# Performance work log

Measured on AMD Instinct MI355X. Metric: run time of the kernel, lower is better.

The kernel has to match this reference:

```python
import jax, jax.numpy as jnp
import numpy as np

# Profile-HMM forward-backward in log space.
# inputs : (M, B, L, S) soft/one-hot observation features
# log_A  : (M, Q, Q) row-stochastic log transition matrix
# log_pi : (M, Q)    log initial distribution
# log_B  : (M, Q, S) log emission matrix

M, B, L, Q, S = 1, 64, 2048, 256, 26
EPS = 1e-16


def setup_inputs() -> dict:
    key = jax.random.key(0)
    k1, k2, k3, k4 = jax.random.split(key, 4)
    inputs = jax.random.uniform(k1, (M, B, L, S), dtype=jnp.float32)
    log_A = jax.nn.log_softmax(jax.random.normal(k2, (M, Q, Q), dtype=jnp.float32), axis=-1)
    log_pi = jax.nn.log_softmax(jax.random.normal(k3, (M, Q), dtype=jnp.float32), axis=-1)
    log_B = jax.nn.log_softmax(jax.random.normal(k4, (M, Q, S), dtype=jnp.float32), axis=-1)
    return {"inputs": inputs, "log_A": log_A, "log_pi": log_pi, "log_B": log_B}


def _forward_backward(inputs, log_A, log_pi, log_B):
    # emission probs per state: e[m,b,l,q] = sum_s inputs[m,b,l,s] * B[m,q,s]
    emit = jnp.einsum('mbls,mqs->mblq', inputs, jnp.exp(log_B))
    log_e = jnp.log(emit + EPS)
    log_e_t = jnp.moveaxis(log_e, 2, 0)  # (L, M, B, Q) time-major

    # forward recursion: alpha_t[i] = logsumexp_j(alpha_{t-1}[j] + A[j,i]) + e_t[i]
    alpha0 = log_pi[:, None, :] + log_e_t[0]  # (M, B, Q)

    def fstep(alpha, le):
        new = jax.nn.logsumexp(alpha[..., :, None] + log_A[:, None], axis=-2) + le
        return new, new

    _, alphas = jax.lax.scan(fstep, alpha0, log_e_t[1:])
    alphas = jnp.concatenate([alpha0[None], alphas], axis=0)  # (L, M, B, Q)

    # backward recursion: beta_t[i] = logsumexp_j(A[i,j] + e_{t+1}[j] + beta_{t+1}[j])
    beta_last = jnp.zeros_like(alpha0)

    def bstep(beta, le):
        new = jax.nn.logsumexp(log_A[:, None] + (le + beta)[:, :, None, :], axis=-1)
        return new, new

    _, betas = jax.lax.scan(bstep, beta_last, log_e_t[1:], reverse=True)
    betas = jnp.concatenate([betas, beta_last[None]], axis=0)  # (L, M, B, Q)

    loglik = jax.nn.logsumexp(alphas[-1], axis=-1)  # (M, B)
    post = alphas + betas - loglik[None, :, :, None]  # state posterior log probs
    return jnp.moveaxis(post, 0, 2), loglik  # (M, B, L, Q), (M, B)


def reference(inputs, log_A, log_pi, log_B):
    post, loglik = _forward_backward(inputs, log_A, log_pi, log_B)
    return post, loglik
```

## Files before the change

### kernel.cpp

```cpp
#include <hip/hip_runtime.h>

namespace {

constexpr int B = 64;
constexpr int L = 2048;
constexpr int Q = 256;
constexpr int S = 26;
constexpr float EPS = 1e-16f;
constexpr size_t POST = (size_t)B * L * Q;

typedef _Float16 h2 __attribute__((ext_vector_type(2)));
typedef _Float16 f16x8 __attribute__((ext_vector_type(8)));
typedef float f32x4 __attribute__((ext_vector_type(4)));

#define MFMA16(a, b, c) __builtin_amdgcn_mfma_f32_16x16x32_f16((a), (b), (c), 0, 0, 0)

struct Smem {
  alignas(16) _Float16 vb[2][Q];
  alignas(16) _Float16 rowh[2][32];
  alignas(16) _Float16 rowl[2][32];
  float sh[2];
  alignas(16) float afin[Q];
};

__device__ __forceinline__ void lds_barrier() {
  asm volatile("s_waitcnt lgkmcnt(0)\n\ts_barrier" ::: "memory");
}

__device__ __forceinline__ float wave_max64(float x) {
#pragma unroll
  for (int off = 32; off > 0; off >>= 1) x = fmaxf(x, __shfl_xor(x, off, 64));
  return x;
}
__device__ __forceinline__ float wave_sum64(float x) {
#pragma unroll
  for (int off = 32; off > 0; off >>= 1) x += __shfl_xor(x, off, 64);
  return x;
}

__device__ __forceinline__ void load_emit_frags(const float* __restrict__ log_B,
                                                int c0, int c1, int g, int q,
                                                f16x8& Bh0, f16x8& Bl0,
                                                f16x8& Bh1, f16x8& Bl1) {
#pragma unroll
  for (int j = 0; j < 8; ++j) {
    const int s = g * 8 + j;
    const float v0 = (s < S) ? __expf(log_B[(size_t)(c0 + q) * S + s]) : 0.f;
    const float v1 = (s < S) ? __expf(log_B[(size_t)(c1 + q) * S + s]) : 0.f;
    const _Float16 h0 = (_Float16)v0, h1 = (_Float16)v1;
    Bh0[j] = h0; Bl0[j] = (_Float16)(v0 - (float)h0);
    Bh1[j] = h1; Bl1[j] = (_Float16)(v1 - (float)h1);
  }
}

__device__ __forceinline__ void stage_row(Smem& sm, int buf, int lane, float2 gg) {
  _Float16 ah = (_Float16)0.f, bh = (_Float16)0.f;
  _Float16 al = (_Float16)0.f, bl = (_Float16)0.f;
  if (lane < 13) {
    ah = (_Float16)gg.x; bh = (_Float16)gg.y;
    al = (_Float16)(gg.x - (float)ah);
    bl = (_Float16)(gg.y - (float)bh);
  }
  ((h2*)sm.rowh[buf])[lane] = h2{ah, bh};
  ((h2*)sm.rowl[buf])[lane] = h2{al, bl};
}

__device__ __forceinline__ void emit_mfma(const f16x8& xh, const f16x8& xl,
                                          const f16x8& Bh0, const f16x8& Bl0,
                                          const f16x8& Bh1, const f16x8& Bl1,
                                          f32x4& E0, f32x4& E1) {
  const f32x4 Z = {0.f, 0.f, 0.f, 0.f};
  E0 = MFMA16(xh, Bl0, Z);
  E0 = MFMA16(xl, Bh0, E0);
  E0 = MFMA16(xh, Bh0, E0);
  E1 = MFMA16(xh, Bl1, Z);
  E1 = MFMA16(xl, Bh1, E1);
  E1 = MFMA16(xh, Bh1, E1);
}

__device__ __forceinline__ void matvec_mfma(const f16x8* va, const f16x8* T0,
                                            const f16x8* T1, float& x0, float& x1) {
  const f32x4 Z = {0.f, 0.f, 0.f, 0.f};
  f32x4 X0a = MFMA16(va[0], T0[0], Z);
  f32x4 X1a = MFMA16(va[0], T1[0], Z);
  f32x4 X0b = MFMA16(va[4], T0[4], Z);
  f32x4 X1b = MFMA16(va[4], T1[4], Z);
#pragma unroll
  for (int f = 1; f < 4; ++f) {
    X0a = MFMA16(va[f], T0[f], X0a);
    X1a = MFMA16(va[f], T1[f], X1a);
    X0b = MFMA16(va[f + 4], T0[f + 4], X0b);
    X1b = MFMA16(va[f + 4], T1[f + 4], X1b);
  }
  x0 = X0a[0] + X0b[0];
  x1 = X1a[0] + X1b[0];
}

__device__ __forceinline__ void read_frags(Smem& sm, int p, int g,
                                           f16x8& xh, f16x8& xl, f16x8* va) {
  xh = *(const f16x8*)(sm.rowh[p] + g * 8);
  xl = *(const f16x8*)(sm.rowl[p] + g * 8);
  const _Float16* vbp = sm.vb[p];
#pragma unroll
  for (int f = 0; f < 8; ++f) va[f] = *(const f16x8*)(vbp + f * 32 + g * 8);
}

__device__ __forceinline__ void fwd_impl(int b, const float* __restrict__ inputs,
                                         const float* __restrict__ log_A,
                                         const float* __restrict__ log_pi,
                                         const float* __restrict__ log_B,
                                         float* __restrict__ out, Smem& sm) {
  const int tid = threadIdx.x, w = tid >> 6, lane = tid & 63;
  const int g = lane >> 4, q = lane & 15;
  const int c0 = w * 32, c1 = c0 + 16;
  const bool rdl = (q == 0);
  const bool epi = (lane < 16);
  const bool stg = (w == 0) && (lane < 16);

  f16x8 T0[8], T1[8];
#pragma unroll
  for (int f = 0; f < 8; ++f) {
#pragma unroll
    for (int j = 0; j < 8; ++j) {
      const int k = f * 32 + g * 8 + j;
      T0[f][j] = (_Float16)__expf(log_A[(size_t)k * Q + c0 + q]);
      T1[f][j] = (_Float16)__expf(log_A[(size_t)k * Q + c1 + q]);
    }
  }
  f16x8 Bh0, Bl0, Bh1, Bl1;
  load_emit_frags(log_B, c0, c1, g, q, Bh0, Bl0, Bh1, Bl1);

  const float2* __restrict__ inp2 = (const float2*)(inputs + (size_t)b * L * S);
  float* __restrict__ post_b = out + (size_t)b * L * Q;

  float2 gHold = {0.f, 0.f};
  if (stg) {
    float2 g0 = {0.f, 0.f}, g1 = {0.f, 0.f};
    if (lane < 13) {
      g0 = inp2[lane];
      g1 = inp2[13 + lane];
      gHold = inp2[26 + lane];
    }
    stage_row(sm, 1, lane, g0);
    stage_row(sm, 0, lane, g1);
  }
  __syncthreads();

  f16x8 xh = {}, xl = {};
  f16x8 va[8];
#pragma unroll
  for (int f = 0; f < 8; ++f) va[f] = f16x8{};

  if (rdl) {
    xh = *(const f16x8*)(sm.rowh[1] + g * 8);
    xl = *(const f16x8*)(sm.rowl[1] + g * 8);
  }
  f32x4 E0, E1;
  emit_mfma(xh, xl, Bh0, Bl0, Bh1, Bl1, E0, E1);
  float zh0 = 1.f, zh1 = 1.f, rdp_h = 0.f;
  if (epi) {
    zh0 = (E0[0] + EPS) * __expf(log_pi[c0 + lane]);
    zh1 = (E1[0] + EPS) * __expf(log_pi[c1 + lane]);
  }
  if (tid == 0) sm.sh[0] = __logf(zh0);
  __syncthreads();
  float rd_prev = sm.sh[0];
  if (epi) {
    const float sc = __expf(-rd_prev);
    sm.vb[0][c0 + lane] = (_Float16)(zh0 * sc);
    sm.vb[0][c1 + lane] = (_Float16)(zh1 * sc);
  }
  __syncthreads();

  int p = 0;
  for (int t = 1; t < L; ++t) {
    if (stg) stage_row(sm, p ^ 1, lane, gHold);
    const float rd = sm.sh[p];
    float2 gN = gHold;
    const int tt = (t + 2 < L) ? t + 2 : L - 1;
    if (w == 0 && lane < 13) gN = inp2[(size_t)tt * 13 + lane];
    if (epi) {
      const float a0 = __logf(zh0) + rdp_h;
      const float a1 = __logf(zh1) + rdp_h;
      post_b[(size_t)(t - 1) * Q + c0 + lane] = a0;
      post_b[(size_t)(t - 1) * Q + c1 + lane] = a1;
    }
    if (rdl) read_frags(sm, p, g, xh, xl, va);
    f32x4 E0_, E1_;
    emit_mfma(xh, xl, Bh0, Bl0, Bh1, Bl1, E0_, E1_);
    float x0, x1;
    matvec_mfma(va, T0, T1, x0, x1);
    const float gam = __expf(rd_prev - rd);
    if (epi) {
      const float e0 = E0_[0] + EPS, e1 = E1_[0] + EPS;
      const float z0 = x0 * e0, z1 = x1 * e1;
      sm.vb[p ^ 1][c0 + lane] = (_Float16)(z0 * gam);
      sm.vb[p ^ 1][c1 + lane] = (_Float16)(z1 * gam);
      if (tid == 0) sm.sh[p ^ 1] = __logf(z0) + rd_prev;
      zh0 = z0; zh1 = z1;
    }
    gHold = gN;
    rdp_h = rd_prev;
    rd_prev = rd;
    lds_barrier();
    p ^= 1;
  }

  if (epi) {
    const float a0 = __logf(zh0) + rdp_h;
    const float a1 = __logf(zh1) + rdp_h;
    post_b[(size_t)(L - 1) * Q + c0 + lane] = a0;
    post_b[(size_t)(L - 1) * Q + c1 + lane] = a1;
    sm.afin[c0 + lane] = a0;
    sm.afin[c1 + lane] = a1;
  }
  __syncthreads();
  if (w == 0) {
    float4 fa = ((const float4*)sm.afin)[lane];
    float m = fmaxf(fmaxf(fa.x, fa.y), fmaxf(fa.z, fa.w));
    m = wave_max64(m);
    float ss = __expf(fa.x - m) + __expf(fa.y - m) + __expf(fa.z - m) + __expf(fa.w - m);
    ss = wave_sum64(ss);
    if (lane == 0) out[POST + b] = __logf(ss) + m;
  }
}

template <int MODE>
__device__ __forceinline__ void bwd_impl(int b, const float* __restrict__ inputs,
                                         const float* __restrict__ log_A,
                                         const float* __restrict__ log_B,
                                         float* __restrict__ out,
                                         float* __restrict__ ws, Smem& sm) {
  const int tid = threadIdx.x, w = tid >> 6, lane = tid & 63;
  const int g = lane >> 4, q = lane & 15;
  const int c0 = w * 32, c1 = c0 + 16;
  const bool rdl = (q == 0);
  const bool epi = (lane < 16);
  const bool stg = (w == 0) && (lane < 16);

  f16x8 T0[8], T1[8];
#pragma unroll
  for (int f = 0; f < 8; ++f) {
#pragma unroll
    for (int j = 0; j < 8; ++j) {
      const int k = f * 32 + g * 8 + j;
      T0[f][j] = (_Float16)__expf(log_A[(size_t)(c0 + q) * Q + k]);
      T1[f][j] = (_Float16)__expf(log_A[(size_t)(c1 + q) * Q + k]);
    }
  }
  f16x8 Bh0, Bl0, Bh1, Bl1;
  load_emit_frags(log_B, c0, c1, g, q, Bh0, Bl0, Bh1, Bl1);

  const float2* __restrict__ inp2 = (const float2*)(inputs + (size_t)b * L * S);
  float* __restrict__ post_b = out + (size_t)b * L * Q;
  float* __restrict__ ws_b = ws + (size_t)b * L * Q;

  float ll = 0.f, a_h0 = 0.f, a_h1 = 0.f;
  if (MODE == 1) {
    ll = out[POST + b];
    if (epi) {
      a_h0 = post_b[(size_t)(L - 1) * Q + c0 + lane];
      a_h1 = post_b[(size_t)(L - 1) * Q + c1 + lane];
    }
  }

  float2 gHold = {0.f, 0.f};
  if (stg) {
    float2 g0 = {0.f, 0.f}, g1 = {0.f, 0.f};
    if (lane < 13) {
      g0 = inp2[(size_t)(L - 1) * 13 + lane];
      g1 = inp2[(size_t)(L - 2) * 13 + lane];
      gHold = inp2[(size_t)(L - 3) * 13 + lane];
    }
    stage_row(sm, 1, lane, g0);
    stage_row(sm, 0, lane, g1);
  }
  __syncthreads();

  f16x8 xh = {}, xl = {};
  f16x8 va[8];
#pragma unroll
  for (int f = 0; f < 8; ++f) va[f] = f16x8{};

  if (rdl) {
    xh = *(const f16x8*)(sm.rowh[1] + g * 8);
    xl = *(const f16x8*)(sm.rowl[1] + g * 8);
  }
  f32x4 E0, E1;
  emit_mfma(xh, xl, Bh0, Bl0, Bh1, Bl1, E0, E1);
  float e0i = 1.f, e1i = 1.f;
  if (epi) { e0i = E0[0] + EPS; e1i = E1[0] + EPS; }
  if (tid == 0) sm.sh[0] = __logf(e0i);
  __syncthreads();
  float rd_prev = sm.sh[0];
  if (epi) {
    const float sc = __expf(-rd_prev);
    sm.vb[0][c0 + lane] = (_Float16)(e0i * sc);
    sm.vb[0][c1 + lane] = (_Float16)(e1i * sc);
  }
  float rh0 = 1.f, rh1 = 1.f, rdp_h = 0.f;
  __syncthreads();

  int p = 0;
  for (int t = L - 2; t >= 0; --t) {
    if (stg) stage_row(sm, p ^ 1, lane, gHold);
    const float rd = sm.sh[p];
    float2 gN = gHold;
    const int tt = (t >= 2) ? t - 2 : 0;
    if (w == 0 && lane < 13) gN = inp2[(size_t)tt * 13 + lane];
    if (epi) {
      const float b0 = __logf(rh0) + rdp_h;
      const float b1 = __logf(rh1) + rdp_h;
      if (MODE == 0) {
        ws_b[(size_t)(t + 1) * Q + c0 + lane] = b0;
        ws_b[(size_t)(t + 1) * Q + c1 + lane] = b1;
      } else {
        post_b[(size_t)(t + 1) * Q + c0 + lane] = a_h0 + b0 - ll;
        post_b[(size_t)(t + 1) * Q + c1 + lane] = a_h1 + b1 - ll;
        a_h0 = post_b[(size_t)t * Q + c0 + lane];
        a_h1 = post_b[(size_t)t * Q + c1 + lane];
      }
    }
    if (rdl) read_frags(sm, p, g, xh, xl, va);
    f32x4 E0_, E1_;
    emit_mfma(xh, xl, Bh0, Bl0, Bh1, Bl1, E0_, E1_);
    float r0, r1;
    matvec_mfma(va, T0, T1, r0, r1);
    const float gam = __expf(rd_prev - rd);
    if (epi) {
      const float e0 = E0_[0] + EPS, e1 = E1_[0] + EPS;
      const float z0 = r0 * e0, z1 = r1 * e1;
      sm.vb[p ^ 1][c0 + lane] = (_Float16)(z0 * gam);
      sm.vb[p ^ 1][c1 + lane] = (_Float16)(z1 * gam);
      if (tid == 0) sm.sh[p ^ 1] = __logf(z0) + rd_prev;
      rh0 = r0; rh1 = r1;
    }
    gHold = gN;
    rdp_h = rd_prev;
    rd_prev = rd;
    lds_barrier();
    p ^= 1;
  }

  if (epi) {
    const float b0 = __logf(rh0) + rdp_h;
    const float b1 = __logf(rh1) + rdp_h;
    if (MODE == 0) {
      ws_b[c0 + lane] = b0;
      ws_b[c1 + lane] = b1;
    } else {
      post_b[c0 + lane] = a_h0 + b0 - ll;
      post_b[c1 + lane] = a_h1 + b1 - ll;
    }
  }
}

__global__ __launch_bounds__(512, 2)
void hmm_fwdbwd(const float* __restrict__ inputs, const float* __restrict__ log_A,
                const float* __restrict__ log_pi, const float* __restrict__ log_B,
                float* __restrict__ out, float* __restrict__ ws) {
  __shared__ Smem sm;
  if (blockIdx.x < B) fwd_impl(blockIdx.x, inputs, log_A, log_pi, log_B, out, sm);
  else                bwd_impl<0>(blockIdx.x - B, inputs, log_A, log_B, out, ws, sm);
}

__global__ __launch_bounds__(256)
void hmm_combine(const float* __restrict__ ws, float* __restrict__ out) {
  const size_t idx = (size_t)blockIdx.x * 256 + threadIdx.x;
  const int b = (int)(idx >> 17);
  const float ll = out[POST + b];
  float4 a = ((const float4*)out)[idx];
  const float4 be = ((const float4*)ws)[idx];
  a.x += be.x - ll;
  a.y += be.y - ll;
  a.z += be.z - ll;
  a.w += be.w - ll;
  ((float4*)out)[idx] = a;
}

__global__ __launch_bounds__(512, 2)
void hmm_fwd_only(const float* __restrict__ inputs, const float* __restrict__ log_A,
                  const float* __restrict__ log_pi, const float* __restrict__ log_B,
                  float* __restrict__ out) {
  __shared__ Smem sm;
  fwd_impl(blockIdx.x, inputs, log_A, log_pi, log_B, out, sm);
}

__global__ __launch_bounds__(512, 2)
void hmm_bwd_fused(const float* __restrict__ inputs, const float* __restrict__ log_A,
                   const float* __restrict__ log_B, float* __restrict__ out) {
  __shared__ Smem sm;
  bwd_impl<1>(blockIdx.x, inputs, log_A, log_B, out, nullptr, sm);
}

}

extern "C" void kernel_launch(void* const* d_in, const int* in_sizes, int n_in,
                              void* d_out, int out_size, void* d_ws, size_t ws_size,
                              hipStream_t stream) {
  const float* inputs = (const float*)d_in[0];
  const float* log_A  = (const float*)d_in[1];
  const float* log_pi = (const float*)d_in[2];
  const float* log_B  = (const float*)d_in[3];
  float* out = (float*)d_out;
  float* ws  = (float*)d_ws;

  if (ws_size >= POST * sizeof(float)) {
    hipLaunchKernelGGL(hmm_fwdbwd, dim3(2 * B), dim3(512), 0, stream,
                       inputs, log_A, log_pi, log_B, out, ws);
    hipLaunchKernelGGL(hmm_combine, dim3((unsigned)(POST / 4 / 256)), dim3(256), 0, stream,
                       ws, out);
  } else {
    hipLaunchKernelGGL(hmm_fwd_only, dim3(B), dim3(512), 0, stream,
                       inputs, log_A, log_pi, log_B, out);
    hipLaunchKernelGGL(hmm_bwd_fused, dim3(B), dim3(512), 0, stream,
                       inputs, log_A, log_B, out);
  }
}
```

Before: 1.601 ms.

## Software-pipeline emission MFMA one step ahead and shorten matvec dependency chains

Computes the emission probabilities for step t+1 during step t, so the emit MFMAs sit off the critical recurrence path and the product uses the value computed in the previous iteration. The prologue loads the first two input rows straight from global memory, converts them in registers, and drops one __syncthreads, and the staged-row prefetch now runs one step further ahead. The matvec is split into four independent accumulation chains of two MFMAs instead of two chains of four, cutting serial MFMA latency. Pointer-increment addressing replaces per-step index arithmetic. The cost is extra live registers for the pipelined values and a more intricate prologue.

```diff
diff --git a/kernel.cpp b/kernel.cpp
--- a/kernel.cpp
+++ b/kernel.cpp
@@ -63,6 +63,25 @@
   }
   ((h2*)sm.rowh[buf])[lane] = h2{ah, bh};
   ((h2*)sm.rowl[buf])[lane] = h2{al, bl};
+}
+
+__device__ __forceinline__ void load_row(const float2* __restrict__ r2, int g,
+                                         bool rdl, float2* ld) {
+  if (rdl) {
+    const float2* p = r2 + g * 4;
+    ld[0] = p[0];
+    if (g < 3) { ld[1] = p[1]; ld[2] = p[2]; ld[3] = p[3]; }
+  }
+}
+
+__device__ __forceinline__ void cvt_row(const float2* ld, f16x8& xh, f16x8& xl) {
+#pragma unroll
+  for (int i = 0; i < 4; ++i) {
+    const float a = ld[i].x, bb = ld[i].y;
+    const _Float16 ah = (_Float16)a, bh = (_Float16)bb;
+    xh[2 * i] = ah;     xl[2 * i] = (_Float16)(a - (float)ah);
+    xh[2 * i + 1] = bh; xl[2 * i + 1] = (_Float16)(bb - (float)bh);
+  }
 }
 
 __device__ __forceinline__ void emit_mfma(const f16x8& xh, const f16x8& xl,
@@ -78,22 +97,19 @@
   E1 = MFMA16(xh, Bh1, E1);
 }
 
-__device__ __forceinline__ void matvec_mfma(const f16x8* va, const f16x8* T0,
-                                            const f16x8* T1, float& x0, float& x1) {
+__device__ __forceinline__ void matvec2(const f16x8* va, const f16x8* T0,
+                                        const f16x8* T1, float& x0, float& x1) {
   const f32x4 Z = {0.f, 0.f, 0.f, 0.f};
-  f32x4 X0a = MFMA16(va[0], T0[0], Z);
-  f32x4 X1a = MFMA16(va[0], T1[0], Z);
-  f32x4 X0b = MFMA16(va[4], T0[4], Z);
-  f32x4 X1b = MFMA16(va[4], T1[4], Z);
-#pragma unroll
-  for (int f = 1; f < 4; ++f) {
-    X0a = MFMA16(va[f], T0[f], X0a);
-    X1a = MFMA16(va[f], T1[f], X1a);
-    X0b = MFMA16(va[f + 4], T0[f + 4], X0b);
-    X1b = MFMA16(va[f + 4], T1[f + 4], X1b);
-  }
-  x0 = X0a[0] + X0b[0];
-  x1 = X1a[0] + X1b[0];
+  f32x4 a0 = MFMA16(va[0], T0[0], Z); a0 = MFMA16(va[1], T0[1], a0);
+  f32x4 b0 = MFMA16(va[2], T0[2], Z); b0 = MFMA16(va[3], T0[3], b0);
+  f32x4 c0 = MFMA16(va[4], T0[4], Z); c0 = MFMA16(va[5], T0[5], c0);
+  f32x4 d0 = MFMA16(va[6], T0[6], Z); d0 = MFMA16(va[7], T0[7], d0);
+  f32x4 a1 = MFMA16(va[0], T1[0], Z); a1 = MFMA16(va[1], T1[1], a1);
+  f32x4 b1 = MFMA16(va[2], T1[2], Z); b1 = MFMA16(va[3], T1[3], b1);
+  f32x4 c1 = MFMA16(va[4], T1[4], Z); c1 = MFMA16(va[5], T1[5], c1);
+  f32x4 d1 = MFMA16(va[6], T1[6], Z); d1 = MFMA16(va[7], T1[7], d1);
+  x0 = (a0[0] + b0[0]) + (c0[0] + d0[0]);
+  x1 = (a1[0] + b1[0]) + (c1[0] + d1[0]);
 }
 
 __device__ __forceinline__ void read_frags(Smem& sm, int p, int g,
@@ -131,32 +147,27 @@
   load_emit_frags(log_B, c0, c1, g, q, Bh0, Bl0, Bh1, Bl1);
 
   const float2* __restrict__ inp2 = (const float2*)(inputs + (size_t)b * L * S);
+  const float2* __restrict__ rlast = inp2 + (size_t)(L - 1) * 13;
   float* __restrict__ post_b = out + (size_t)b * L * Q;
 
-  float2 gHold = {0.f, 0.f};
-  if (stg) {
-    float2 g0 = {0.f, 0.f}, g1 = {0.f, 0.f};
-    if (lane < 13) {
-      g0 = inp2[lane];
-      g1 = inp2[13 + lane];
-      gHold = inp2[26 + lane];
-    }
-    stage_row(sm, 1, lane, g0);
-    stage_row(sm, 0, lane, g1);
-  }
-  __syncthreads();
+  float2 r0v[4] = {}, r1v[4] = {};
+  load_row(inp2, g, rdl, r0v);
+  load_row(inp2 + 13, g, rdl, r1v);
+  float2 g2 = {0.f, 0.f}, gHold = {0.f, 0.f};
+  if (w == 0 && lane < 13) { g2 = inp2[26 + lane]; gHold = inp2[39 + lane]; }
+  if (stg) stage_row(sm, 0, lane, g2);
 
   f16x8 xh = {}, xl = {};
-  f16x8 va[8];
-#pragma unroll
-  for (int f = 0; f < 8; ++f) va[f] = f16x8{};
-
-  if (rdl) {
-    xh = *(const f16x8*)(sm.rowh[1] + g * 8);
-    xl = *(const f16x8*)(sm.rowl[1] + g * 8);
-  }
+  cvt_row(r0v, xh, xl);
   f32x4 E0, E1;
   emit_mfma(xh, xl, Bh0, Bl0, Bh1, Bl1, E0, E1);
+  float eP0, eP1;
+  {
+    cvt_row(r1v, xh, xl);
+    f32x4 F0, F1;
+    emit_mfma(xh, xl, Bh0, Bl0, Bh1, Bl1, F0, F1);
+    eP0 = F0[0] + EPS; eP1 = F1[0] + EPS;
+  }
   float zh0 = 1.f, zh1 = 1.f, rdp_h = 0.f;
   if (epi) {
     zh0 = (E0[0] + EPS) * __expf(log_pi[c0 + lane]);
@@ -172,33 +183,38 @@
   }
   __syncthreads();
 
+  f16x8 va[8];
+#pragma unroll
+  for (int f = 0; f < 8; ++f) va[f] = f16x8{};
+
+  const float2* pin = inp2 + 4 * 13;
+  float* pb = post_b + c0 + lane;
   int p = 0;
   for (int t = 1; t < L; ++t) {
     if (stg) stage_row(sm, p ^ 1, lane, gHold);
     const float rd = sm.sh[p];
+    if (rdl) read_frags(sm, p, g, xh, xl, va);
     float2 gN = gHold;
-    const int tt = (t + 2 < L) ? t + 2 : L - 1;
-    if (w == 0 && lane < 13) gN = inp2[(size_t)tt * 13 + lane];
+    if (w == 0 && lane < 13) gN = ((t + 3 < L) ? pin : rlast)[lane];
+    pin += 13;
     if (epi) {
-      const float a0 = __logf(zh0) + rdp_h;
-      const float a1 = __logf(zh1) + rdp_h;
-      post_b[(size_t)(t - 1) * Q + c0 + lane] = a0;
-      post_b[(size_t)(t - 1) * Q + c1 + lane] = a1;
-    }
-    if (rdl) read_frags(sm, p, g, xh, xl, va);
-    f32x4 E0_, E1_;
-    emit_mfma(xh, xl, Bh0, Bl0, Bh1, Bl1, E0_, E1_);
+      pb[0]  = __logf(zh0) + rdp_h;
+      pb[16] = __logf(zh1) + rdp_h;
+    }
+    pb += Q;
+    f32x4 F0_, F1_;
+    emit_mfma(xh, xl, Bh0, Bl0, Bh1, Bl1, F0_, F1_);
     float x0, x1;
-    matvec_mfma(va, T0, T1, x0, x1);
+    matvec2(va, T0, T1, x0, x1);
     const float gam = __expf(rd_prev - rd);
     if (epi) {
-      const float e0 = E0_[0] + EPS, e1 = E1_[0] + EPS;
-      const float z0 = x0 * e0, z1 = x1 * e1;
+      const float z0 = x0 * eP0, z1 = x1 * eP1;
       sm.vb[p ^ 1][c0 + lane] = (_Float16)(z0 * gam);
       sm.vb[p ^ 1][c1 + lane] = (_Float16)(z1 * gam);
       if (tid == 0) sm.sh[p ^ 1] = __logf(z0) + rd_prev;
       zh0 = z0; zh1 = z1;
     }
+    eP0 = F0_[0] + EPS; eP1 = F1_[0] + EPS;
     gHold = gN;
     rdp_h = rd_prev;
     rd_prev = rd;
@@ -209,8 +225,7 @@
   if (epi) {
     const float a0 = __logf(zh0) + rdp_h;
     const float a1 = __logf(zh1) + rdp_h;
-    post_b[(size_t)(L - 1) * Q + c0 + lane] = a0;
-    post_b[(size_t)(L - 1) * Q + c1 + lane] = a1;
+    pb[0] = a0; pb[16] = a1;
     sm.afin[c0 + lane] = a0;
     sm.afin[c1 + lane] = a1;
   }
@@ -264,30 +279,27 @@
     }
   }
 
-  float2 gHold = {0.f, 0.f};
-  if (stg) {
-    float2 g0 = {0.f, 0.f}, g1 = {0.f, 0.f};
-    if (lane < 13) {
-      g0 = inp2[(size_t)(L - 1) * 13 + lane];
-      g1 = inp2[(size_t)(L - 2) * 13 + lane];
-      gHold = inp2[(size_t)(L - 3) * 13 + lane];
-    }
-    stage_row(sm, 1, lane, g0);
-    stage_row(sm, 0, lane, g1);
-  }
-  __syncthreads();
+  float2 rAv[4] = {}, rBv[4] = {};
+  load_row(inp2 + (size_t)(L - 1) * 13, g, rdl, rAv);
+  load_row(inp2 + (size_t)(L - 2) * 13, g, rdl, rBv);
+  float2 g2 = {0.f, 0.f}, gHold = {0.f, 0.f};
+  if (w == 0 && lane < 13) {
+    g2 = inp2[(size_t)(L - 3) * 13 + lane];
+    gHold = inp2[(size_t)(L - 4) * 13 + lane];
+  }
+  if (stg) stage_row(sm, 0, lane, g2);
 
   f16x8 xh = {}, xl = {};
-  f16x8 va[8];
-#pragma unroll
-  for (int f = 0; f < 8; ++f) va[f] = f16x8{};
-
-  if (rdl) {
-    xh = *(const f16x8*)(sm.rowh[1] + g * 8);
-    xl = *(const f16x8*)(sm.rowl[1] + g * 8);
-  }
+  cvt_row(rAv, xh, xl);
   f32x4 E0, E1;
   emit_mfma(xh, xl, Bh0, Bl0, Bh1, Bl1, E0, E1);
+  float eP0, eP1;
+  {
+    cvt_row(rBv, xh, xl);
+    f32x4 F0, F1;
+    emit_mfma(xh, xl, Bh0, Bl0, Bh1, Bl1, F0, F1);
+    eP0 = F0[0] + EPS; eP1 = F1[0] + EPS;
+  }
   float e0i = 1.f, e1i = 1.f;
   if (epi) { e0i = E0[0] + EPS; e1i = E1[0] + EPS; }
   if (tid == 0) sm.sh[0] = __logf(e0i);
@@ -301,40 +313,47 @@
   float rh0 = 1.f, rh1 = 1.f, rdp_h = 0.f;
   __syncthreads();
 
+  f16x8 va[8];
+#pragma unroll
+  for (int f = 0; f < 8; ++f) va[f] = f16x8{};
+
+  const float2* pin = inp2 + (size_t)(L - 5) * 13;
+  float* wp = ws_b + (size_t)(L - 1) * Q + c0 + lane;
+  float* pp = post_b + (size_t)(L - 1) * Q + c0 + lane;
   int p = 0;
   for (int t = L - 2; t >= 0; --t) {
     if (stg) stage_row(sm, p ^ 1, lane, gHold);
     const float rd = sm.sh[p];
+    if (rdl) read_frags(sm, p, g, xh, xl, va);
     float2 gN = gHold;
-    const int tt = (t >= 2) ? t - 2 : 0;
-    if (w == 0 && lane < 13) gN = inp2[(size_t)tt * 13 + lane];
+    if (w == 0 && lane < 13) gN = ((t >= 3) ? pin : inp2)[lane];
+    pin -= 13;
     if (epi) {
       const float b0 = __logf(rh0) + rdp_h;
       const float b1 = __logf(rh1) + rdp_h;
       if (MODE == 0) {
-        ws_b[(size_t)(t + 1) * Q + c0 + lane] = b0;
-        ws_b[(size_t)(t + 1) * Q + c1 + lane] = b1;
+        wp[0] = b0; wp[16] = b1;
       } else {
-        post_b[(size_t)(t + 1) * Q + c0 + lane] = a_h0 + b0 - ll;
-        post_b[(size_t)(t + 1) * Q + c1 + lane] = a_h1 + b1 - ll;
-        a_h0 = post_b[(size_t)t * Q + c0 + lane];
-        a_h1 = post_b[(size_t)t * Q + c1 + lane];
+        pp[0] = a_h0 + b0 - ll;
+        pp[16] = a_h1 + b1 - ll;
+        a_h0 = (pp - Q)[0];
+        a_h1 = (pp - Q)[16];
       }
     }
-    if (rdl) read_frags(sm, p, g, xh, xl, va);
-    f32x4 E0_, E1_;
-    emit_mfma(xh, xl, Bh0, Bl0, Bh1, Bl1, E0_, E1_);
+    wp -= Q; pp -= Q;
+    f32x4 F0_, F1_;
+    emit_mfma(xh, xl, Bh0, Bl0, Bh1, Bl1, F0_, F1_);
     float r0, r1;
-    matvec_mfma(va, T0, T1, r0, r1);
+    matvec2(va, T0, T1, r0, r1);
     const float gam = __expf(rd_prev - rd);
     if (epi) {
-      const float e0 = E0_[0] + EPS, e1 = E1_[0] + EPS;
-      const float z0 = r0 * e0, z1 = r1 * e1;
+      const float z0 = r0 * eP0, z1 = r1 * eP1;
       sm.vb[p ^ 1][c0 + lane] = (_Float16)(z0 * gam);
       sm.vb[p ^ 1][c1 + lane] = (_Float16)(z1 * gam);
       if (tid == 0) sm.sh[p ^ 1] = __logf(z0) + rd_prev;
       rh0 = r0; rh1 = r1;
     }
+    eP0 = F0_[0] + EPS; eP1 = F1_[0] + EPS;
     gHold = gN;
     rdp_h = rd_prev;
     rd_prev = rd;
@@ -346,11 +365,10 @@
     const float b0 = __logf(rh0) + rdp_h;
     const float b1 = __logf(rh1) + rdp_h;
     if (MODE == 0) {
-      ws_b[c0 + lane] = b0;
-      ws_b[c1 + lane] = b1;
+      wp[0] = b0; wp[16] = b1;
     } else {
-      post_b[c0 + lane] = a_h0 + b0 - ll;
-      post_b[c1 + lane] = a_h1 + b1 - ll;
+      pp[0] = a_h0 + b0 - ll;
+      pp[16] = a_h1 + b1 - ll;
     }
   }
 }
```

New measurement: 1.683 ms. 5.1% more time.

## Precompute emissions in separate parallel kernel before forward/backward recursion

Applied to the files above, without the earlier changes.

Adds an hmm_emit kernel that computes all emission probabilities with split-fp16 MFMA across 256 blocks and stores them as fp16 in workspace. The forward/backward recursion kernels then only load the precomputed per-timestep emissions, which removes the per-step emission matmul from the serial critical path. The path runs only when the workspace holds 6 bytes per posterior element. It costs an extra launch and a round trip of the emission tensor through global memory, and fp16 storage with a clamp at 6e-5 changes precision for very small emissions.

```diff
diff --git a/kernel.cpp b/kernel.cpp
--- a/kernel.cpp
+++ b/kernel.cpp
@@ -14,6 +14,332 @@
 typedef float f32x4 __attribute__((ext_vector_type(4)));
 
 #define MFMA16(a, b, c) __builtin_amdgcn_mfma_f32_16x16x32_f16((a), (b), (c), 0, 0, 0)
+
+
+__device__ __forceinline__ void lds_barrier() {
+  asm volatile("s_waitcnt lgkmcnt(0)\n\ts_barrier" ::: "memory");
+}
+
+__device__ __forceinline__ float wave_max64(float x) {
+#pragma unroll
+  for (int off = 32; off > 0; off >>= 1) x = fmaxf(x, __shfl_xor(x, off, 64));
+  return x;
+}
+__device__ __forceinline__ float wave_sum64(float x) {
+#pragma unroll
+  for (int off = 32; off > 0; off >>= 1) x += __shfl_xor(x, off, 64);
+  return x;
+}
+
+
+struct SmemE {
+  alignas(16) _Float16 vb[2][Q];
+  float sh[2];
+  alignas(16) float afin[Q];
+};
+
+__device__ __forceinline__ void matvec2(const f16x8* va, const f16x8* T0,
+                                        const f16x8* T1, float& x0, float& x1) {
+  const f32x4 Z = {0.f, 0.f, 0.f, 0.f};
+  f32x4 a0 = MFMA16(va[0], T0[0], Z); a0 = MFMA16(va[1], T0[1], a0);
+  f32x4 b0 = MFMA16(va[2], T0[2], Z); b0 = MFMA16(va[3], T0[3], b0);
+  f32x4 c0 = MFMA16(va[4], T0[4], Z); c0 = MFMA16(va[5], T0[5], c0);
+  f32x4 d0 = MFMA16(va[6], T0[6], Z); d0 = MFMA16(va[7], T0[7], d0);
+  f32x4 a1 = MFMA16(va[0], T1[0], Z); a1 = MFMA16(va[1], T1[1], a1);
+  f32x4 b1 = MFMA16(va[2], T1[2], Z); b1 = MFMA16(va[3], T1[3], b1);
+  f32x4 c1 = MFMA16(va[4], T1[4], Z); c1 = MFMA16(va[5], T1[5], c1);
+  f32x4 d1 = MFMA16(va[6], T1[6], Z); d1 = MFMA16(va[7], T1[7], d1);
+  x0 = (a0[0] + b0[0]) + (c0[0] + d0[0]);
+  x1 = (a1[0] + b1[0]) + (c1[0] + d1[0]);
+}
+
+__device__ __forceinline__ void read_va(SmemE& sm, int p, int g, f16x8* va) {
+  const _Float16* vbp = sm.vb[p];
+#pragma unroll
+  for (int f = 0; f < 8; ++f) va[f] = *(const f16x8*)(vbp + f * 32 + g * 8);
+}
+
+__global__ __launch_bounds__(512)
+void hmm_emit(const float* __restrict__ inputs, const float* __restrict__ log_B,
+              _Float16* __restrict__ eall) {
+  const int tid = threadIdx.x, w = tid >> 6, lane = tid & 63;
+  const int g = lane >> 4, q = lane & 15;
+  const int b = blockIdx.x >> 2, quar = blockIdx.x & 3;
+  const float* __restrict__ inp = inputs + (size_t)b * L * S;
+  _Float16* __restrict__ eb = eall + (size_t)b * L * Q;
+
+  const int tbase = (quar * 32 + w * 4) * 16;
+  f16x8 xh[4], xl[4];
+#pragma unroll
+  for (int i = 0; i < 4; ++i) {
+    const int trow = tbase + i * 16 + q;
+    const float* rp = inp + (size_t)trow * S;
+    float v[8];
+#pragma unroll
+    for (int j = 0; j < 8; ++j) {
+      const int s = g * 8 + j;
+      v[j] = (s < S) ? rp[s] : 0.f;
+    }
+#pragma unroll
+    for (int j = 0; j < 8; ++j) {
+      const _Float16 h = (_Float16)v[j];
+      xh[i][j] = h;
+      xl[i][j] = (_Float16)(v[j] - (float)h);
+    }
+  }
+  for (int k = 0; k < 16; ++k) {
+    f16x8 Bh, Bl;
+#pragma unroll
+    for (int j = 0; j < 8; ++j) {
+      const int s = g * 8 + j;
+      const float vv = (s < S) ? __expf(log_B[(size_t)(k * 16 + q) * S + s]) : 0.f;
+      const _Float16 h = (_Float16)vv;
+      Bh[j] = h;
+      Bl[j] = (_Float16)(vv - (float)h);
+    }
+    const f32x4 Z = {0.f, 0.f, 0.f, 0.f};
+#pragma unroll
+    for (int i = 0; i < 4; ++i) {
+      f32x4 E = MFMA16(xh[i], Bl, Z);
+      E = MFMA16(xl[i], Bh, E);
+      E = MFMA16(xh[i], Bh, E);
+      const int t0 = tbase + i * 16 + (lane >> 4) * 4;
+      const int col = k * 16 + (lane & 15);
+#pragma unroll
+      for (int r = 0; r < 4; ++r) {
+        const float ev = fmaxf(E[r] + EPS, 6.0e-5f);
+        eb[(size_t)(t0 + r) * Q + col] = (_Float16)ev;
+      }
+    }
+  }
+}
+
+__device__ __forceinline__ void fwd_e(int b, const _Float16* __restrict__ eall,
+                                      const float* __restrict__ log_A,
+                                      const float* __restrict__ log_pi,
+                                      float* __restrict__ out, SmemE& sm) {
+  const int tid = threadIdx.x, w = tid >> 6, lane = tid & 63;
+  const int g = lane >> 4, q = lane & 15;
+  const int c0 = w * 32, c1 = c0 + 16;
+  const bool rdl = (q == 0);
+  const bool epi = (lane < 16);
+
+  f16x8 T0[8], T1[8];
+#pragma unroll
+  for (int f = 0; f < 8; ++f) {
+#pragma unroll
+    for (int j = 0; j < 8; ++j) {
+      const int k = f * 32 + g * 8 + j;
+      T0[f][j] = (_Float16)__expf(log_A[(size_t)k * Q + c0 + q]);
+      T1[f][j] = (_Float16)__expf(log_A[(size_t)k * Q + c1 + q]);
+    }
+  }
+
+  const _Float16* __restrict__ eb = eall + (size_t)b * L * Q;
+  float* __restrict__ post_b = out + (size_t)b * L * Q;
+  const _Float16* e0p = eb + c0 + lane;
+
+  float ez0 = 1.f, ez1 = 1.f;
+  float e1a = 1.f, e1b = 1.f, e2a = 1.f, e2b = 1.f;
+  float e3a = 1.f, e3b = 1.f, e0a = 1.f, e0b = 1.f;
+  if (epi) {
+    ez0 = (float)e0p[0];        ez1 = (float)e0p[16];
+    e1a = (float)e0p[1 * Q];    e1b = (float)e0p[1 * Q + 16];
+    e2a = (float)e0p[2 * Q];    e2b = (float)e0p[2 * Q + 16];
+    e3a = (float)e0p[3 * Q];    e3b = (float)e0p[3 * Q + 16];
+    e0a = (float)e0p[4 * Q];    e0b = (float)e0p[4 * Q + 16];
+  }
+
+  float zh0 = 1.f, zh1 = 1.f, rdp_h = 0.f;
+  if (epi) {
+    zh0 = ez0 * __expf(log_pi[c0 + lane]);
+    zh1 = ez1 * __expf(log_pi[c1 + lane]);
+  }
+  if (tid == 0) sm.sh[0] = __logf(zh0);
+  __syncthreads();
+  float rd_prev = sm.sh[0];
+  if (epi) {
+    const float sc = __expf(-rd_prev);
+    sm.vb[0][c0 + lane] = (_Float16)(zh0 * sc);
+    sm.vb[0][c1 + lane] = (_Float16)(zh1 * sc);
+  }
+  __syncthreads();
+
+  f16x8 va[8];
+#pragma unroll
+  for (int f = 0; f < 8; ++f) va[f] = f16x8{};
+
+  const _Float16* ep = eb + (size_t)5 * Q + c0 + lane;
+  const _Float16* epLast = eb + (size_t)(L - 1) * Q + c0 + lane;
+  float* pb = post_b + c0 + lane;
+  int p = 0;
+
+  auto step = [&](float& eX0, float& eX1) {
+    const float rd = sm.sh[p];
+    if (rdl) read_va(sm, p, g, va);
+    if (epi) {
+      pb[0] = __logf(zh0) + rdp_h;
+      pb[16] = __logf(zh1) + rdp_h;
+    }
+    pb += Q;
+    float x0, x1;
+    matvec2(va, T0, T1, x0, x1);
+    const float gam = __expf(rd_prev - rd);
+    if (epi) {
+      const float z0 = x0 * eX0, z1 = x1 * eX1;
+      sm.vb[p ^ 1][c0 + lane] = (_Float16)(z0 * gam);
+      sm.vb[p ^ 1][c1 + lane] = (_Float16)(z1 * gam);
+      if (tid == 0) sm.sh[p ^ 1] = __logf(z0) + rd_prev;
+      zh0 = z0; zh1 = z1;
+      const _Float16* pe = (ep <= epLast) ? ep : epLast;
+      eX0 = (float)pe[0];
+      eX1 = (float)pe[16];
+    }
+    ep += Q;
+    rdp_h = rd_prev;
+    rd_prev = rd;
+    lds_barrier();
+    p ^= 1;
+  };
+
+  int t = 1;
+  for (; t + 3 < L; t += 4) {
+    step(e1a, e1b);
+    step(e2a, e2b);
+    step(e3a, e3b);
+    step(e0a, e0b);
+  }
+  step(e1a, e1b);
+  step(e2a, e2b);
+  step(e3a, e3b);
+
+  if (epi) {
+    const float a0 = __logf(zh0) + rdp_h;
+    const float a1 = __logf(zh1) + rdp_h;
+    pb[0] = a0; pb[16] = a1;
+    sm.afin[c0 + lane] = a0;
+    sm.afin[c1 + lane] = a1;
+  }
+  __syncthreads();
+  if (w == 0) {
+    float4 fa = ((const float4*)sm.afin)[lane];
+    float m = fmaxf(fmaxf(fa.x, fa.y), fmaxf(fa.z, fa.w));
+    m = wave_max64(m);
+    float ss = __expf(fa.x - m) + __expf(fa.y - m) + __expf(fa.z - m) + __expf(fa.w - m);
+    ss = wave_sum64(ss);
+    if (lane == 0) out[POST + b] = __logf(ss) + m;
+  }
+}
+
+__device__ __forceinline__ void bwd_e(int b, const _Float16* __restrict__ eall,
+                                      const float* __restrict__ log_A,
+                                      float* __restrict__ ws, SmemE& sm) {
+  const int tid = threadIdx.x, w = tid >> 6, lane = tid & 63;
+  const int g = lane >> 4, q = lane & 15;
+  const int c0 = w * 32, c1 = c0 + 16;
+  const bool rdl = (q == 0);
+  const bool epi = (lane < 16);
+
+  f16x8 T0[8], T1[8];
+#pragma unroll
+  for (int f = 0; f < 8; ++f) {
+#pragma unroll
+    for (int j = 0; j < 8; ++j) {
+      const int k = f * 32 + g * 8 + j;
+      T0[f][j] = (_Float16)__expf(log_A[(size_t)(c0 + q) * Q + k]);
+      T1[f][j] = (_Float16)__expf(log_A[(size_t)(c1 + q) * Q + k]);
+    }
+  }
+
+  const _Float16* __restrict__ eb = eall + (size_t)b * L * Q;
+  float* __restrict__ ws_b = ws + (size_t)b * L * Q;
+  const _Float16* eLp = eb + (size_t)(L - 1) * Q + c0 + lane;
+
+  float ez0 = 1.f, ez1 = 1.f;
+  float e1a = 1.f, e1b = 1.f, e2a = 1.f, e2b = 1.f;
+  float e3a = 1.f, e3b = 1.f, e0a = 1.f, e0b = 1.f;
+  if (epi) {
+    ez0 = (float)eLp[0];            ez1 = (float)eLp[16];
+    e1a = (float)eLp[-1 * Q];       e1b = (float)eLp[-1 * Q + 16];
+    e2a = (float)eLp[-2 * Q];       e2b = (float)eLp[-2 * Q + 16];
+    e3a = (float)eLp[-3 * Q];       e3b = (float)eLp[-3 * Q + 16];
+    e0a = (float)eLp[-4 * Q];       e0b = (float)eLp[-4 * Q + 16];
+  }
+
+  if (tid == 0) sm.sh[0] = __logf(ez0);
+  __syncthreads();
+  float rd_prev = sm.sh[0];
+  if (epi) {
+    const float sc = __expf(-rd_prev);
+    sm.vb[0][c0 + lane] = (_Float16)(ez0 * sc);
+    sm.vb[0][c1 + lane] = (_Float16)(ez1 * sc);
+  }
+  float rh0 = 1.f, rh1 = 1.f, rdp_h = 0.f;
+  __syncthreads();
+
+  f16x8 va[8];
+#pragma unroll
+  for (int f = 0; f < 8; ++f) va[f] = f16x8{};
+
+  const _Float16* ep = eb + (size_t)(L - 6) * Q + c0 + lane;
+  const _Float16* epFirst = eb + c0 + lane;
+  float* wp = ws_b + (size_t)(L - 1) * Q + c0 + lane;
+  int p = 0;
+
+  auto step = [&](float& eX0, float& eX1) {
+    const float rd = sm.sh[p];
+    if (rdl) read_va(sm, p, g, va);
+    if (epi) {
+      wp[0] = __logf(rh0) + rdp_h;
+      wp[16] = __logf(rh1) + rdp_h;
+    }
+    wp -= Q;
+    float x0, x1;
+    matvec2(va, T0, T1, x0, x1);
+    const float gam = __expf(rd_prev - rd);
+    if (epi) {
+      const float z0 = x0 * eX0, z1 = x1 * eX1;
+      sm.vb[p ^ 1][c0 + lane] = (_Float16)(z0 * gam);
+      sm.vb[p ^ 1][c1 + lane] = (_Float16)(z1 * gam);
+      if (tid == 0) sm.sh[p ^ 1] = __logf(z0) + rd_prev;
+      rh0 = x0; rh1 = x1;
+      const _Float16* pe = (ep >= epFirst) ? ep : epFirst;
+      eX0 = (float)pe[0];
+      eX1 = (float)pe[16];
+    }
+    ep -= Q;
+    rdp_h = rd_prev;
+    rd_prev = rd;
+    lds_barrier();
+    p ^= 1;
+  };
+
+  int t = L - 2;
+  for (; t >= 3; t -= 4) {
+    step(e1a, e1b);
+    step(e2a, e2b);
+    step(e3a, e3b);
+    step(e0a, e0b);
+  }
+  step(e1a, e1b);
+  step(e2a, e2b);
+  step(e3a, e3b);
+
+  if (epi) {
+    wp[0] = __logf(rh0) + rdp_h;
+    wp[16] = __logf(rh1) + rdp_h;
+  }
+}
+
+__global__ __launch_bounds__(512, 2)
+void hmm_fwdbwd_e(const _Float16* __restrict__ eall, const float* __restrict__ log_A,
+                  const float* __restrict__ log_pi, float* __restrict__ out,
+                  float* __restrict__ ws) {
+  __shared__ SmemE sm;
+  if (blockIdx.x < B) fwd_e(blockIdx.x, eall, log_A, log_pi, out, sm);
+  else                bwd_e(blockIdx.x - B, eall, log_A, ws, sm);
+}
+
 
 struct Smem {
   alignas(16) _Float16 vb[2][Q];
@@ -22,21 +348,6 @@
   float sh[2];
   alignas(16) float afin[Q];
 };
-
-__device__ __forceinline__ void lds_barrier() {
-  asm volatile("s_waitcnt lgkmcnt(0)\n\ts_barrier" ::: "memory");
-}
-
-__device__ __forceinline__ float wave_max64(float x) {
-#pragma unroll
-  for (int off = 32; off > 0; off >>= 1) x = fmaxf(x, __shfl_xor(x, off, 64));
-  return x;
-}
-__device__ __forceinline__ float wave_sum64(float x) {
-#pragma unroll
-  for (int off = 32; off > 0; off >>= 1) x += __shfl_xor(x, off, 64);
-  return x;
-}
 
 __device__ __forceinline__ void load_emit_frags(const float* __restrict__ log_B,
                                                 int c0, int c1, int g, int q,
@@ -405,11 +716,22 @@
   float* out = (float*)d_out;
   float* ws  = (float*)d_ws;
 
-  if (ws_size >= POST * sizeof(float)) {
+  const size_t needA = POST * 6;
+  const size_t needB = POST * sizeof(float);
+
+  if (ws_size >= needA) {
+    _Float16* eall = (_Float16*)(ws + POST);
+    hipLaunchKernelGGL(hmm_emit, dim3(4 * B), dim3(512), 0, stream,
+                       inputs, log_B, eall);
+    hipLaunchKernelGGL(hmm_fwdbwd_e, dim3(2 * B), dim3(512), 0, stream,
+                       eall, log_A, log_pi, out, ws);
+    hipLaunchKernelGGL(hmm_combine, dim3((unsigned)(POST / 4 / 256)), dim3(256), 0,
+                       stream, ws, out);
+  } else if (ws_size >= needB) {
     hipLaunchKernelGGL(hmm_fwdbwd, dim3(2 * B), dim3(512), 0, stream,
                        inputs, log_A, log_pi, log_B, out, ws);
-    hipLaunchKernelGGL(hmm_combine, dim3((unsigned)(POST / 4 / 256)), dim3(256), 0, stream,
-                       ws, out);
+    hipLaunchKernelGGL(hmm_combine, dim3((unsigned)(POST / 4 / 256)), dim3(256), 0,
+                       stream, ws, out);
   } else {
     hipLaunchKernelGGL(hmm_fwd_only, dim3(B), dim3(512), 0, stream,
                        inputs, log_A, log_pi, log_B, out);
```

New measurement: 1.817 ms. +13.5%, slower.
